# Performance work log

Measured on AMD Instinct MI355X. Metric: run time of the kernel, lower is better.

## Reference

```python
import jax, jax.numpy as jnp
import numpy as np

KH, KW = 5, 5  # kernel_size
B, C, H, W = 4, 3, 1024, 1024


def setup_inputs() -> dict:
    key = jax.random.key(0)
    x = jax.random.normal(key, (B, C, H, W), dtype=jnp.float32)
    return {"input": x}


def _median_blur(x, kh, kw):
    # zero padding identical to _compute_zero_padding: (k-1)//2 per side -> 'same' output
    ph, pw = (kh - 1) // 2, (kw - 1) // 2
    b, c, h, w = x.shape
    xp = jnp.pad(x, ((0, 0), (0, 0), (ph, ph), (pw, pw)))
    # Materialize the kh*kw shifted views (same math as conv2d with binary kernel / im2col)
    patches = jnp.stack(
        [xp[:, :, i:i + h, j:j + w] for i in range(kh) for j in range(kw)],
        axis=2,
    )  # [B, C, kh*kw, H, W]
    # torch.median(dim=2)[0]: for odd kh*kw this is the exact middle order statistic
    sorted_p = jnp.sort(patches, axis=2)
    mid = (kh * kw - 1) // 2
    return sorted_p[:, :, mid, :, :]


def reference(input) -> jnp.ndarray:
    return _median_blur(input, KH, KW)
```

## Files before the change

kernel.cpp:

```cpp
#include <hip/hip_runtime.h>

#define CAS(a, b) { float _t = fminf(a, b); (b) = fmaxf(a, b); (a) = _t; }
#define MED3(a,b,c) __builtin_amdgcn_fmed3f((a),(b),(c))

#define IMG    1024
#define TW     128
#define TH     8
#define RAW_W  136

#define SWZ(P) ((P) ^ ((((P) >> 4) & 1) << 3) ^ ((((P) >> 5) & 1) << 2))

__device__ __forceinline__ void sort5(float& a0, float& a1, float& a2, float& a3, float& a4) {
    CAS(a0, a1); CAS(a3, a4); CAS(a2, a4); CAS(a2, a3);
    CAS(a0, a3); CAS(a0, a2); CAS(a1, a4); CAS(a1, a3); CAS(a1, a2);
}

__device__ __forceinline__ float tail13v(const float* cd) {
    float e0 = cd[0],  e1 = cd[1];
    float f0 = cd[2],  f1 = cd[3],  f2 = cd[4];
    float h0 = cd[5],  h1 = cd[6],  h2 = cd[7];
    float g0 = cd[8],  g1 = cd[9],  g2 = cd[10];
    float k0 = cd[11], k1 = cd[12];

    float A0 = fminf(e0, f0), M = fmaxf(e0, f0);
    float A4 = f2;
    float A3 = fmaxf(e1, f1);
    float A1 = fminf(fminf(M, e1), f1);
    float A2 = MED3(e1, f1, M);
    float C0 = g0;
    float C4 = fmaxf(g2, k1);
    float C1 = fminf(g1, k0);
    float mgk = fminf(g2, k1);
    float C3 = fmaxf(fmaxf(mgk, g1), k0);
    float C2 = MED3(g1, k0, mgk);
    float r3 = fmaxf(fmaxf(fmaxf(fminf(A0, C3), fminf(A1, C2)), fminf(A2, C1)), fminf(A3, C0));
    float r4 = fmaxf(fmaxf(fmaxf(fminf(A0, C4), fminf(A1, C3)), fminf(A2, C2)),
                     fmaxf(fminf(A3, C1), fminf(A4, C0)));
    float r5 = fmaxf(fmaxf(fmaxf(fminf(A1, C4), fminf(A2, C3)), fminf(A3, C2)),
                     fmaxf(fmaxf(fminf(A4, C1), A0), C0));
    float r6 = fmaxf(fmaxf(fmaxf(fminf(A2, C4), fminf(A3, C3)), fminf(A4, C2)),
                     fmaxf(A1, C1));
    return fmaxf(fmaxf(fmaxf(fminf(r4, h2), fminf(r5, h1)), fminf(r6, h0)), r3);
}

__global__ __launch_bounds__(256, 6)
void median5x5_kernel(const float* __restrict__ in, float* __restrict__ out) {
    __shared__ float scol[5][TH][RAW_W];

    const int tx  = threadIdx.x;
    const int ty  = threadIdx.y;
    const int x0  = blockIdx.x * TW;
    const int y0  = blockIdx.y * TH;
    const float* plane = in + (size_t)blockIdx.z * (IMG * IMG);
    const int gy0 = y0 + ty - 2;

    auto ldp = [&](int gy, int gxb) -> float2 {
        float2 v = make_float2(0.f, 0.f);
        if ((unsigned)gy < IMG && (unsigned)gxb < IMG)
            v = *(const float2*)(plane + (size_t)gy * IMG + gxb);
        return v;
    };

#define TASK(p) { \
        int gxb = x0 - 2 + 2 * (p); \
        float2 r0 = ldp(gy0 + 0, gxb); \
        float2 r1 = ldp(gy0 + 1, gxb); \
        float2 r2 = ldp(gy0 + 2, gxb); \
        float2 r3 = ldp(gy0 + 3, gxb); \
        float2 r4 = ldp(gy0 + 4, gxb); \
        sort5(r0.x, r1.x, r2.x, r3.x, r4.x); \
        sort5(r0.y, r1.y, r2.y, r3.y, r4.y); \
        int cs = 2 * SWZ((p) + 1); \
        *(float2*)&scol[0][ty][cs] = r0; \
        *(float2*)&scol[1][ty][cs] = r1; \
        *(float2*)&scol[2][ty][cs] = r2; \
        *(float2*)&scol[3][ty][cs] = r3; \
        *(float2*)&scol[4][ty][cs] = r4; }
    TASK(tx);
    TASK(tx + 32);
    if (tx < 2) TASK(tx + 64);
#undef TASK
    __syncthreads();

    const int P0 = 2 * tx + 1;
    const int o0 = 2 * SWZ(P0 + 0);
    const int o1 = 2 * SWZ(P0 + 1);
    const int o2 = 2 * SWZ(P0 + 2);
    const int o3 = 2 * SWZ(P0 + 3);
    float cd[4][13];

    #pragma unroll
    for (int i = 0; i < 5; ++i) {
        const float* rp = &scol[i][ty][0];
        float2 u0 = *(const float2*)(rp + o0);
        float2 u1 = *(const float2*)(rp + o1);
        float2 u2 = *(const float2*)(rp + o2);
        float2 u3 = *(const float2*)(rp + o3);
        float c0 = u0.x, c1 = u0.y, c2 = u1.x, c3 = u1.y;
        float c4 = u2.x, c5 = u2.y, c6 = u3.x, c7 = u3.y;

        float m0 = c3, m1 = c4; CAS(m0, m1);
        float a = c1, b = c2; CAS(a, b);
        float s0 = fminf(a, m0), t1 = fmaxf(a, m0);
        float t2 = fminf(b, m1), s3 = fmaxf(b, m1);
        float s1 = fminf(t1, t2), s2 = fmaxf(t1, t2);
        float d = c5, e = c6; CAS(d, e);
        float q0 = fminf(m0, d), w1 = fmaxf(m0, d);
        float w2 = fminf(m1, e), q3 = fmaxf(m1, e);
        float q1 = fminf(w1, w2), q2 = fmaxf(w1, w2);

#define EXT(px, S0, S1, S2, S3, X) { \
        if (i == 0)      { cd[px][0]  = MED3(S2, S3, X); cd[px][1]  = fmaxf(S3, X); } \
        else if (i == 1) { cd[px][2]  = MED3(S1, S2, X); cd[px][3]  = MED3(S2, S3, X); cd[px][4] = fmaxf(S3, X); } \
        else if (i == 2) { cd[px][5]  = MED3(S0, S1, X); cd[px][6]  = MED3(S1, S2, X); cd[px][7] = MED3(S2, S3, X); } \
        else if (i == 3) { cd[px][8]  = fminf(S0, X);    cd[px][9]  = MED3(S0, S1, X); cd[px][10] = MED3(S1, S2, X); } \
        else             { cd[px][11] = fminf(S0, X);    cd[px][12] = MED3(S0, S1, X); } }
        EXT(0, s0, s1, s2, s3, c0)
        EXT(1, s0, s1, s2, s3, c5)
        EXT(2, q0, q1, q2, q3, c2)
        EXT(3, q0, q1, q2, q3, c7)
#undef EXT
    }

    float4 o;
    o.x = tail13v(cd[0]);
    o.y = tail13v(cd[1]);
    o.z = tail13v(cd[2]);
    o.w = tail13v(cd[3]);
    *(float4*)(out + (size_t)blockIdx.z * (IMG * IMG) + (size_t)(y0 + ty) * IMG + x0 + 4 * tx) = o;
}

extern "C" void kernel_launch(void* const* d_in, const int* in_sizes, int n_in,
                              void* d_out, int out_size, void* d_ws, size_t ws_size,
                              hipStream_t stream) {
    const float* in  = (const float*)d_in[0];
    float*       out = (float*)d_out;
    dim3 block(32, TH, 1);
    dim3 grid(IMG / TW, IMG / TH, 12);
    hipLaunchKernelGGL(median5x5_kernel, grid, block, 0, stream, in, out);
}
```

Before: 137.0 us.

## Shrink tile to 64 columns with two outputs per thread

Halves the tile width to 64 columns, so each thread computes two adjacent output pixels instead of four. The shared-memory column swizzle is dropped, a smaller shared buffer is used, and the launch-bounds occupancy hint drops from 6 to 4. The goal is lower register pressure per thread and a simpler sorting network over the middle four columns. The cost is less reuse of the shared partial sorts across neighbouring pixels, so more ALU work per output, plus twice as many blocks.

Measured after the change: 141.6 us. 3.4% more time.

```diff
diff --git a/kernel.cpp b/kernel.cpp
--- a/kernel.cpp
+++ b/kernel.cpp
@@ -3,12 +3,10 @@
 #define CAS(a, b) { float _t = fminf(a, b); (b) = fmaxf(a, b); (a) = _t; }
 #define MED3(a,b,c) __builtin_amdgcn_fmed3f((a),(b),(c))
 
-#define IMG    1024
-#define TW     128
-#define TH     8
-#define RAW_W  136
-
-#define SWZ(P) ((P) ^ ((((P) >> 4) & 1) << 3) ^ ((((P) >> 5) & 1) << 2))
+#define IMG 1024
+#define TW  64
+#define TH  8
+#define SW  72
 
 __device__ __forceinline__ void sort5(float& a0, float& a1, float& a2, float& a3, float& a4) {
     CAS(a0, a1); CAS(a3, a4); CAS(a2, a4); CAS(a2, a3);
@@ -43,9 +41,9 @@
     return fmaxf(fmaxf(fmaxf(fminf(r4, h2), fminf(r5, h1)), fminf(r6, h0)), r3);
 }
 
-__global__ __launch_bounds__(256, 6)
+__global__ __launch_bounds__(256, 4)
 void median5x5_kernel(const float* __restrict__ in, float* __restrict__ out) {
-    __shared__ float scol[5][TH][RAW_W];
+    __shared__ float scol[5][TH][SW];
 
     const int tx  = threadIdx.x;
     const int ty  = threadIdx.y;
@@ -70,64 +68,47 @@
         float2 r4 = ldp(gy0 + 4, gxb); \
         sort5(r0.x, r1.x, r2.x, r3.x, r4.x); \
         sort5(r0.y, r1.y, r2.y, r3.y, r4.y); \
-        int cs = 2 * SWZ((p) + 1); \
+        int cs = 2 * (p); \
         *(float2*)&scol[0][ty][cs] = r0; \
         *(float2*)&scol[1][ty][cs] = r1; \
         *(float2*)&scol[2][ty][cs] = r2; \
         *(float2*)&scol[3][ty][cs] = r3; \
         *(float2*)&scol[4][ty][cs] = r4; }
     TASK(tx);
-    TASK(tx + 32);
-    if (tx < 2) TASK(tx + 64);
+    if (tx < 2) TASK(tx + 32);
 #undef TASK
     __syncthreads();
 
-    const int P0 = 2 * tx + 1;
-    const int o0 = 2 * SWZ(P0 + 0);
-    const int o1 = 2 * SWZ(P0 + 1);
-    const int o2 = 2 * SWZ(P0 + 2);
-    const int o3 = 2 * SWZ(P0 + 3);
-    float cd[4][13];
+    const int cb = 2 * tx;
+    float cd[2][13];
 
     #pragma unroll
     for (int i = 0; i < 5; ++i) {
-        const float* rp = &scol[i][ty][0];
-        float2 u0 = *(const float2*)(rp + o0);
-        float2 u1 = *(const float2*)(rp + o1);
-        float2 u2 = *(const float2*)(rp + o2);
-        float2 u3 = *(const float2*)(rp + o3);
+        const float* rp = &scol[i][ty][cb];
+        float2 u0 = *(const float2*)(rp);
+        float2 u1 = *(const float2*)(rp + 2);
+        float2 u2 = *(const float2*)(rp + 4);
         float c0 = u0.x, c1 = u0.y, c2 = u1.x, c3 = u1.y;
-        float c4 = u2.x, c5 = u2.y, c6 = u3.x, c7 = u3.y;
+        float c4 = u2.x, c5 = u2.y;
 
-        float m0 = c3, m1 = c4; CAS(m0, m1);
-        float a = c1, b = c2; CAS(a, b);
-        float s0 = fminf(a, m0), t1 = fmaxf(a, m0);
-        float t2 = fminf(b, m1), s3 = fmaxf(b, m1);
-        float s1 = fminf(t1, t2), s2 = fmaxf(t1, t2);
-        float d = c5, e = c6; CAS(d, e);
-        float q0 = fminf(m0, d), w1 = fmaxf(m0, d);
-        float w2 = fminf(m1, e), q3 = fmaxf(m1, e);
-        float q1 = fminf(w1, w2), q2 = fmaxf(w1, w2);
+        float m0 = c1, m1 = c2, m2 = c3, m3 = c4;
+        CAS(m0, m1); CAS(m2, m3); CAS(m0, m2); CAS(m1, m3); CAS(m1, m2);
 
-#define EXT(px, S0, S1, S2, S3, X) { \
-        if (i == 0)      { cd[px][0]  = MED3(S2, S3, X); cd[px][1]  = fmaxf(S3, X); } \
-        else if (i == 1) { cd[px][2]  = MED3(S1, S2, X); cd[px][3]  = MED3(S2, S3, X); cd[px][4] = fmaxf(S3, X); } \
-        else if (i == 2) { cd[px][5]  = MED3(S0, S1, X); cd[px][6]  = MED3(S1, S2, X); cd[px][7] = MED3(S2, S3, X); } \
-        else if (i == 3) { cd[px][8]  = fminf(S0, X);    cd[px][9]  = MED3(S0, S1, X); cd[px][10] = MED3(S1, S2, X); } \
-        else             { cd[px][11] = fminf(S0, X);    cd[px][12] = MED3(S0, S1, X); } }
-        EXT(0, s0, s1, s2, s3, c0)
-        EXT(1, s0, s1, s2, s3, c5)
-        EXT(2, q0, q1, q2, q3, c2)
-        EXT(3, q0, q1, q2, q3, c7)
+#define EXT(px, X) { \
+        if (i == 0)      { cd[px][0]  = MED3(m2, m3, X); cd[px][1]  = fmaxf(m3, X); } \
+        else if (i == 1) { cd[px][2]  = MED3(m1, m2, X); cd[px][3]  = MED3(m2, m3, X); cd[px][4] = fmaxf(m3, X); } \
+        else if (i == 2) { cd[px][5]  = MED3(m0, m1, X); cd[px][6]  = MED3(m1, m2, X); cd[px][7] = MED3(m2, m3, X); } \
+        else if (i == 3) { cd[px][8]  = fminf(m0, X);    cd[px][9]  = MED3(m0, m1, X); cd[px][10] = MED3(m1, m2, X); } \
+        else             { cd[px][11] = fminf(m0, X);    cd[px][12] = MED3(m0, m1, X); } }
+        EXT(0, c0)
+        EXT(1, c5)
 #undef EXT
     }
 
-    float4 o;
+    float2 o;
     o.x = tail13v(cd[0]);
     o.y = tail13v(cd[1]);
-    o.z = tail13v(cd[2]);
-    o.w = tail13v(cd[3]);
-    *(float4*)(out + (size_t)blockIdx.z * (IMG * IMG) + (size_t)(y0 + ty) * IMG + x0 + 4 * tx) = o;
+    *(float2*)(out + (size_t)blockIdx.z * (IMG * IMG) + (size_t)(y0 + ty) * IMG + x0 + 2 * tx) = o;
 }
 
 extern "C" void kernel_launch(void* const* d_in, const int* in_sizes, int n_in,
```
